# Performance work log

Hardware: AMD Instinct MI355X
Metric: run time of the kernel (lower is better)

## Reference

```python
import jax, jax.numpy as jnp
import numpy as np

B, N, K, H = 8, 4096, 32, 256
LN_EPS = 1e-5


def setup_inputs() -> dict:
    key = jax.random.key(0)
    k1, k2, k3, k4, k5 = jax.random.split(key, 5)
    h = jax.random.normal(k1, (B, N, H), dtype=jnp.float32)
    nbr_idx = jax.random.randint(k2, (B, N, K), 0, N, dtype=jnp.int64)
    nbr_w = jax.random.uniform(k3, (B, N, K), dtype=jnp.float32)
    # Linear weights stored torch-style as [out, in]; y = x @ W.T
    W_self = jax.random.normal(k4, (H, H), dtype=jnp.float32) / np.sqrt(H)
    W_neigh = jax.random.normal(k5, (H, H), dtype=jnp.float32) / np.sqrt(H)
    ln_gamma = jnp.ones((H,), dtype=jnp.float32)
    ln_beta = jnp.zeros((H,), dtype=jnp.float32)
    return {"h": h, "nbr_idx": nbr_idx, "nbr_w": nbr_w, "W_self": W_self,
            "W_neigh": W_neigh, "ln_gamma": ln_gamma, "ln_beta": ln_beta}


def _layer_norm(x, gamma, beta):
    mu = jnp.mean(x, axis=-1, keepdims=True)
    var = jnp.mean(jnp.square(x - mu), axis=-1, keepdims=True)
    return (x - mu) * jax.lax.rsqrt(var + LN_EPS) * gamma + beta


def reference(h, nbr_idx, nbr_w, W_self, W_neigh, ln_gamma, ln_beta):
    b, n, hd = h.shape
    k = nbr_idx.shape[2]
    # gather neighbor features: [B, N, k, H]
    flat_idx = nbr_idx.reshape(b, n * k)
    h_nbr = jnp.take_along_axis(h, flat_idx[:, :, None], axis=1).reshape(b, n, k, hd)
    # weighted aggregate over neighbors
    h_agg = jnp.einsum('bnk,bnkh->bnh', nbr_w, h_nbr)
    # dual linear + exact (erf) GELU, matching torch nn.GELU default
    out = jax.nn.gelu(h @ W_self.T + h_agg @ W_neigh.T, approximate=False)
    # dropout is identity in eval mode
    return _layer_norm(out, ln_gamma, ln_beta)
```

## Files before the change

kernel.cpp:

```cpp
#include <hip/hip_runtime.h>
#include <hip/hip_bf16.h>
#include <math.h>
#include <stdint.h>

constexpr int Nn = 4096, Kk = 32, Hh = 256;
constexpr int Mm = 8 * Nn;

typedef float  f32x4 __attribute__((ext_vector_type(4)));
typedef short  s16x8 __attribute__((ext_vector_type(8)));

static __device__ __forceinline__ ushort f2bf(float f) {
  uint32_t u = __float_as_uint(f);
  u += 0x7FFF + ((u >> 16) & 1);
  return (ushort)(u >> 16);
}
static __device__ __forceinline__ float bf2f(ushort s) {
  return __uint_as_float(((uint32_t)s) << 16);
}
static __device__ __forceinline__ void gl_lds16(const ushort* g, ushort* l) {
  __builtin_amdgcn_global_load_lds(
      (const __attribute__((address_space(1))) void*)g,
      (__attribute__((address_space(3))) void*)l, 16, 0, 0);
}
static __device__ __forceinline__ float gelu_t(float x) {
  float u = x * x;
  float y = x * (1.5957691216f + 0.0713548162726f * u);
  float t = __expf(y);
  return x - x * __builtin_amdgcn_rcpf(t + 1.0f);
}

__global__ __launch_bounds__(256) void prep_w(const float* __restrict__ Ws,
                                              const float* __restrict__ Wn,
                                              ushort* __restrict__ Wc,
                                              const int* __restrict__ idxp,
                                              int* __restrict__ flag) {
  if (blockIdx.x == 0 && threadIdx.x < 64) {
    unsigned long long bl = __ballot(idxp[2 * threadIdx.x + 1] != 0);
    if (threadIdx.x == 0) *flag = (bl != 0ULL) ? 1 : 0;
  }
  int i = blockIdx.x * 256 + threadIdx.x;
  int j  = i >> 6;
  int k4 = i & 63;
  const float* src = (j < 256) ? (Ws + (size_t)j * 256 + k4 * 4)
                               : (Wn + (size_t)(j - 256) * 256 + k4 * 4);
  float4 v = *reinterpret_cast<const float4*>(src);
  ushort4 o = { f2bf(v.x), f2bf(v.y), f2bf(v.z), f2bf(v.w) };
  reinterpret_cast<ushort4*>(Wc)[i] = o;
}

__global__ __launch_bounds__(512, 4) void gemm1(const float* __restrict__ h,
                                                const ushort* __restrict__ Wc,
                                                ushort* __restrict__ hs,
                                                ushort* __restrict__ hn) {
  __shared__ ushort lA[2][64 * 64];
  __shared__ ushort lB[2][256 * 64];
  const int tid = threadIdx.x, wid = tid >> 6, lane = tid & 63;
  const int wr = wid >> 1, wc = wid & 1;

  const int blk = blockIdx.x;
  const int b = blk & 7, t = blk >> 3;
  const int nblk = t & 1, mblk = t >> 1;
  const int m0 = b * Nn + mblk * 64;
  const ushort* Wbase = Wc + (size_t)nblk * 256 * 256;

  f32x4 acc[8];
  #pragma unroll
  for (int j = 0; j < 8; ++j) acc[j] = f32x4{0.f, 0.f, 0.f, 0.f};

  float4 a0, a1;
  const int ar = tid >> 3, as = tid & 7;
  auto aload = [&](int kt) {
    const float* src = h + (size_t)(m0 + ar) * 256 + kt * 64 + as * 8;
    a0 = *reinterpret_cast<const float4*>(src);
    a1 = *reinterpret_cast<const float4*>(src + 4);
  };
  auto awrite = [&](int buf) {
    s16x8 u = { (short)f2bf(a0.x), (short)f2bf(a0.y), (short)f2bf(a0.z),
                (short)f2bf(a0.w), (short)f2bf(a1.x), (short)f2bf(a1.y),
                (short)f2bf(a1.z), (short)f2bf(a1.w) };
    *reinterpret_cast<s16x8*>(&lA[buf][ar * 64 + ((as ^ (ar & 7)) << 3)]) = u;
  };
  auto bstage = [&](int buf, int kt) {
    #pragma unroll
    for (int c = 0; c < 4; ++c) {
      int ch = wid + c * 8;
      int r = ch * 8 + (lane >> 3);
      int s = (lane & 7) ^ (r & 7);
      gl_lds16(Wbase + (size_t)r * 256 + kt * 64 + s * 8, &lB[buf][ch * 512]);
    }
  };

  aload(0);
  bstage(0, 0);
  awrite(0);
  __syncthreads();

  int buf = 0;
  for (int kt = 0; kt < 4; ++kt) {
    if (kt < 3) { aload(kt + 1); bstage(buf ^ 1, kt + 1); }
    #pragma unroll
    for (int kk = 0; kk < 2; ++kk) {
      const int ks = kk * 4 + (lane >> 4);
      const int ra = wr * 16 + (lane & 15);
      s16x8 af = *reinterpret_cast<const s16x8*>(
          &lA[buf][ra * 64 + ((ks ^ (ra & 7)) << 3)]);
      s16x8 bfr[8];
      #pragma unroll
      for (int nj = 0; nj < 8; ++nj) {
        int rb = wc * 128 + nj * 16 + (lane & 15);
        bfr[nj] = *reinterpret_cast<const s16x8*>(
            &lB[buf][rb * 64 + ((ks ^ (rb & 7)) << 3)]);
      }
      #pragma unroll
      for (int nj = 0; nj < 8; ++nj)
        acc[nj] = __builtin_amdgcn_mfma_f32_16x16x32_bf16(af, bfr[nj],
                                                          acc[nj], 0, 0, 0);
    }
    if (kt < 3) awrite(buf ^ 1);
    __syncthreads();
    buf ^= 1;
  }

  ushort* dst = (nblk == 0) ? hs : hn;
  #pragma unroll
  for (int nj = 0; nj < 8; ++nj)
    #pragma unroll
    for (int jj = 0; jj < 4; ++jj) {
      int row = wr * 16 + (lane >> 4) * 4 + jj;
      int col = wc * 128 + nj * 16 + (lane & 15);
      dst[(size_t)(m0 + row) * 256 + col] = f2bf(acc[nj][jj]);
    }
}

__global__ __launch_bounds__(512, 4) void k2(const ushort* __restrict__ hs,
                                             const ushort* __restrict__ hn,
                                             const void* __restrict__ idx,
                                             const float* __restrict__ w,
                                             const float* __restrict__ gamma,
                                             const float* __restrict__ beta,
                                             float* __restrict__ out,
                                             const int* __restrict__ flag) {
  const int tid = threadIdx.x, wv = tid >> 6, lane = tid & 63;
  const int hw = lane >> 5, l5 = lane & 31;
  const int b = blockIdx.x & 7;
  const int m = b * Nn + (blockIdx.x >> 3) * 16 + wv * 2 + hw;
  const int is32 = *flag;

  size_t kb = (size_t)m * Kk + l5;
  int   myi = is32 ? ((const int*)idx)[kb] : (int)((const long long*)idx)[kb];
  float myw = w[kb];

  s16x8 hv = *reinterpret_cast<const s16x8*>(hs + (size_t)m * Hh + l5 * 8);
  float4 gm0 = reinterpret_cast<const float4*>(gamma)[l5 * 2];
  float4 gm1 = reinterpret_cast<const float4*>(gamma)[l5 * 2 + 1];
  float4 bt0 = reinterpret_cast<const float4*>(beta)[l5 * 2];
  float4 bt1 = reinterpret_cast<const float4*>(beta)[l5 * 2 + 1];

  const char* hnb = (const char*)(hn + (size_t)b * Nn * Hh);
  const int lb = l5 << 4;

  int o[32];
  #pragma unroll
  for (int k = 0; k < 32; ++k)
    o[k] = (__shfl(myi, k, 32) << 9) + lb;

  f32x4 aA0{0,0,0,0}, aA1{0,0,0,0}, aB0{0,0,0,0}, aB1{0,0,0,0};

#define LD(k) (*reinterpret_cast<const s16x8*>(hnb + o[k]))
#define CONSA(q, wt) { \
    aA0[0] += wt * bf2f((ushort)q[0]); aA0[1] += wt * bf2f((ushort)q[1]); \
    aA0[2] += wt * bf2f((ushort)q[2]); aA0[3] += wt * bf2f((ushort)q[3]); \
    aA1[0] += wt * bf2f((ushort)q[4]); aA1[1] += wt * bf2f((ushort)q[5]); \
    aA1[2] += wt * bf2f((ushort)q[6]); aA1[3] += wt * bf2f((ushort)q[7]); }
#define CONSB(q, wt) { \
    aB0[0] += wt * bf2f((ushort)q[0]); aB0[1] += wt * bf2f((ushort)q[1]); \
    aB0[2] += wt * bf2f((ushort)q[2]); aB0[3] += wt * bf2f((ushort)q[3]); \
    aB1[0] += wt * bf2f((ushort)q[4]); aB1[1] += wt * bf2f((ushort)q[5]); \
    aB1[2] += wt * bf2f((ushort)q[6]); aB1[3] += wt * bf2f((ushort)q[7]); }

  s16x8 p0 = LD(0), p1 = LD(1), p2 = LD(2), p3 = LD(3);

  #pragma unroll
  for (int k = 0; k < 32; k += 4) {
    float w0 = __shfl(myw, k, 32),     w1 = __shfl(myw, k + 1, 32);
    float w2 = __shfl(myw, k + 2, 32), w3 = __shfl(myw, k + 3, 32);
    s16x8 q0 = p0, q1 = p1, q2 = p2, q3 = p3;
    if (k + 4 < 32) {
      p0 = LD(k + 4); p1 = LD(k + 5); p2 = LD(k + 6); p3 = LD(k + 7);
    }
    CONSA(q0, w0); CONSB(q1, w1); CONSA(q2, w2); CONSB(q3, w3);
  }
#undef LD
#undef CONSA
#undef CONSB

  float g[8];
  #pragma unroll
  for (int j = 0; j < 4; ++j) {
    g[j]     = gelu_t(aA0[j] + aB0[j] + bf2f((ushort)hv[j]));
    g[j + 4] = gelu_t(aA1[j] + aB1[j] + bf2f((ushort)hv[j + 4]));
  }

  float sv = 0.f, qv = 0.f;
  #pragma unroll
  for (int j = 0; j < 8; ++j) { sv += g[j]; qv += g[j] * g[j]; }
  #pragma unroll
  for (int msk = 16; msk >= 1; msk >>= 1) {
    sv += __shfl_xor(sv, msk, 64);
    qv += __shfl_xor(qv, msk, 64);
  }
  float mean = sv * (1.0f / 256.0f);
  float var  = qv * (1.0f / 256.0f) - mean * mean;
  float inv  = rsqrtf(var + 1e-5f);

  float4 o0, o1;
  o0.x = (g[0] - mean) * inv * gm0.x + bt0.x;
  o0.y = (g[1] - mean) * inv * gm0.y + bt0.y;
  o0.z = (g[2] - mean) * inv * gm0.z + bt0.z;
  o0.w = (g[3] - mean) * inv * gm0.w + bt0.w;
  o1.x = (g[4] - mean) * inv * gm1.x + bt1.x;
  o1.y = (g[5] - mean) * inv * gm1.y + bt1.y;
  o1.z = (g[6] - mean) * inv * gm1.z + bt1.z;
  o1.w = (g[7] - mean) * inv * gm1.w + bt1.w;
  float4* op = reinterpret_cast<float4*>(out + (size_t)m * Hh + l5 * 8);
  op[0] = o0;
  op[1] = o1;
}

extern "C" void kernel_launch(void* const* d_in, const int* in_sizes, int n_in,
                              void* d_out, int out_size, void* d_ws, size_t ws_size,
                              hipStream_t stream) {
  const float* h     = (const float*)d_in[0];
  const void*  idx   = d_in[1];
  const float* w     = (const float*)d_in[2];
  const float* Ws    = (const float*)d_in[3];
  const float* Wn    = (const float*)d_in[4];
  const float* gamma = (const float*)d_in[5];
  const float* beta  = (const float*)d_in[6];
  float* out = (float*)d_out;

  ushort* hs = (ushort*)d_ws;
  ushort* hn = hs + (size_t)Mm * Hh;
  ushort* Wc = hn + (size_t)Mm * Hh;
  int* flag  = (int*)(Wc + 512 * 256);

  prep_w<<<128, 256, 0, stream>>>(Ws, Wn, Wc, (const int*)idx, flag);
  gemm1<<<1024, 512, 0, stream>>>(h, Wc, hs, hn);
  k2<<<2048, 512, 0, stream>>>(hs, hn, idx, w, gamma, beta, out, flag);
}
```

Before: 58.25 us.

## Split each row's neighbor gather across two half-waves and combine by shuffle

Each wave now handles one output row instead of two, and each half-wave gathers and accumulates 16 of the 32 neighbors. The partial sums are merged with a cross-half xor shuffle before GELU and layer norm, and only the lower half-wave writes the result. Blocks shrink to 256 threads and the grid grows fourfold. This halves the serial gather chain per lane to expose more memory-level parallelism, at the cost of redundant GELU/LN math in the upper half, extra shuffles, and more waves to schedule.

```diff
diff --git a/kernel.cpp b/kernel.cpp
--- a/kernel.cpp
+++ b/kernel.cpp
@@ -132,7 +132,7 @@
     }
 }
 
-__global__ __launch_bounds__(512, 4) void k2(const ushort* __restrict__ hs,
+__global__ __launch_bounds__(256, 4) void k2(const ushort* __restrict__ hs,
                                              const ushort* __restrict__ hn,
                                              const void* __restrict__ idx,
                                              const float* __restrict__ w,
@@ -143,10 +143,10 @@
   const int tid = threadIdx.x, wv = tid >> 6, lane = tid & 63;
   const int hw = lane >> 5, l5 = lane & 31;
   const int b = blockIdx.x & 7;
-  const int m = b * Nn + (blockIdx.x >> 3) * 16 + wv * 2 + hw;
+  const int m = b * Nn + (blockIdx.x >> 3) * 4 + wv;
   const int is32 = *flag;
 
-  size_t kb = (size_t)m * Kk + l5;
+  size_t kb = (size_t)m * Kk + hw * 16 + (l5 & 15);
   int   myi = is32 ? ((const int*)idx)[kb] : (int)((const long long*)idx)[kb];
   float myw = w[kb];
 
@@ -156,17 +156,15 @@
   float4 bt0 = reinterpret_cast<const float4*>(beta)[l5 * 2];
   float4 bt1 = reinterpret_cast<const float4*>(beta)[l5 * 2 + 1];
 
-  const char* hnb = (const char*)(hn + (size_t)b * Nn * Hh);
-  const int lb = l5 << 4;
-
-  int o[32];
-  #pragma unroll
-  for (int k = 0; k < 32; ++k)
-    o[k] = (__shfl(myi, k, 32) << 9) + lb;
+  const ushort* hnb = hn + (size_t)b * Nn * Hh;
+
+  auto ld = [&](int k) -> s16x8 {
+    int r = __shfl(myi, k, 32);
+    return *reinterpret_cast<const s16x8*>(hnb + ((size_t)r << 8) + (l5 << 3));
+  };
 
   f32x4 aA0{0,0,0,0}, aA1{0,0,0,0}, aB0{0,0,0,0}, aB1{0,0,0,0};
 
-#define LD(k) (*reinterpret_cast<const s16x8*>(hnb + o[k]))
 #define CONSA(q, wt) { \
     aA0[0] += wt * bf2f((ushort)q[0]); aA0[1] += wt * bf2f((ushort)q[1]); \
     aA0[2] += wt * bf2f((ushort)q[2]); aA0[3] += wt * bf2f((ushort)q[3]); \
@@ -178,28 +176,34 @@
     aB1[0] += wt * bf2f((ushort)q[4]); aB1[1] += wt * bf2f((ushort)q[5]); \
     aB1[2] += wt * bf2f((ushort)q[6]); aB1[3] += wt * bf2f((ushort)q[7]); }
 
-  s16x8 p0 = LD(0), p1 = LD(1), p2 = LD(2), p3 = LD(3);
-
-  #pragma unroll
-  for (int k = 0; k < 32; k += 4) {
+  s16x8 p0 = ld(0), p1 = ld(1), p2 = ld(2), p3 = ld(3);
+
+  #pragma unroll
+  for (int k = 0; k < 16; k += 4) {
     float w0 = __shfl(myw, k, 32),     w1 = __shfl(myw, k + 1, 32);
     float w2 = __shfl(myw, k + 2, 32), w3 = __shfl(myw, k + 3, 32);
     s16x8 q0 = p0, q1 = p1, q2 = p2, q3 = p3;
-    if (k + 4 < 32) {
-      p0 = LD(k + 4); p1 = LD(k + 5); p2 = LD(k + 6); p3 = LD(k + 7);
+    if (k + 4 < 16) {
+      p0 = ld(k + 4); p1 = ld(k + 5); p2 = ld(k + 6); p3 = ld(k + 7);
     }
     CONSA(q0, w0); CONSB(q1, w1); CONSA(q2, w2); CONSB(q3, w3);
   }
-#undef LD
 #undef CONSA
 #undef CONSB
 
   float g[8];
   #pragma unroll
   for (int j = 0; j < 4; ++j) {
-    g[j]     = gelu_t(aA0[j] + aB0[j] + bf2f((ushort)hv[j]));
-    g[j + 4] = gelu_t(aA1[j] + aB1[j] + bf2f((ushort)hv[j + 4]));
-  }
+    g[j]     = aA0[j] + aB0[j];
+    g[j + 4] = aA1[j] + aB1[j];
+  }
+  #pragma unroll
+  for (int j = 0; j < 8; ++j)
+    g[j] += __shfl_xor(g[j], 32, 64);
+
+  #pragma unroll
+  for (int j = 0; j < 8; ++j)
+    g[j] = gelu_t(g[j] + bf2f((ushort)hv[j]));
 
   float sv = 0.f, qv = 0.f;
   #pragma unroll
@@ -222,9 +226,11 @@
   o1.y = (g[5] - mean) * inv * gm1.y + bt1.y;
   o1.z = (g[6] - mean) * inv * gm1.z + bt1.z;
   o1.w = (g[7] - mean) * inv * gm1.w + bt1.w;
-  float4* op = reinterpret_cast<float4*>(out + (size_t)m * Hh + l5 * 8);
-  op[0] = o0;
-  op[1] = o1;
+  if (hw == 0) {
+    float4* op = reinterpret_cast<float4*>(out + (size_t)m * Hh + l5 * 8);
+    op[0] = o0;
+    op[1] = o1;
+  }
 }
 
 extern "C" void kernel_launch(void* const* d_in, const int* in_sizes, int n_in,
@@ -246,5 +252,5 @@
 
   prep_w<<<128, 256, 0, stream>>>(Ws, Wn, Wc, (const int*)idx, flag);
   gemm1<<<1024, 512, 0, stream>>>(h, Wc, hs, hn);
-  k2<<<2048, 512, 0, stream>>>(hs, hn, idx, w, gamma, beta, out, flag);
-}
+  k2<<<8192, 256, 0, stream>>>(hs, hn, idx, w, gamma, beta, out, flag);
+}
```

Result: no change. 59.01 us (+1.3%).
